# Kernel optimization log

Hardware: AMD Instinct MI355X
Metric: run time of the kernel (lower is better)

Reference implementation:

```python
import jax, jax.numpy as jnp
import numpy as np

B, C, H, NP, M = 32, 768, 12, 196, 64
D = C // H
GRID = 14  # sqrt(196)
NG = 1 + NP  # cls + patches = 197
EPS = 1e-5


def _ln(x, w, b):
    mu = x.mean(-1, keepdims=True)
    var = ((x - mu) ** 2).mean(-1, keepdims=True)
    return (x - mu) * jax.lax.rsqrt(var + EPS) * w + b


def setup_inputs() -> dict:
    key = jax.random.key(0)
    ks = jax.random.split(key, 14)
    std = 0.02
    return {
        "x": jax.random.normal(ks[0], (B, NG + M, C), dtype=jnp.float32),
        "ps": jax.random.uniform(ks[1], (B, M, 2), dtype=jnp.float32) * 224.0,
        "ns": jax.random.randint(ks[2], (B,), 1, M + 1, dtype=jnp.int32),
        "norm1_w": jnp.ones((C,), jnp.float32),
        "norm1_b": jnp.zeros((C,), jnp.float32),
        "qkv_w": jax.random.normal(ks[3], (3 * C, C), jnp.float32) * std,
        "proj_w": jax.random.normal(ks[4], (C, C), jnp.float32) * std,
        "proj_b": jnp.zeros((C,), jnp.float32),
        "norm2_w": jnp.ones((C,), jnp.float32),
        "norm2_b": jnp.zeros((C,), jnp.float32),
        "fc1_w": jax.random.normal(ks[5], (4 * C, C), jnp.float32) * std,
        "fc1_b": jnp.zeros((4 * C,), jnp.float32),
        "fc2_w": jax.random.normal(ks[6], (C, 4 * C), jnp.float32) * std,
        "fc2_b": jnp.zeros((C,), jnp.float32),
    }


def reference(x, ps, ns, norm1_w, norm1_b, qkv_w, proj_w, proj_b,
              norm2_w, norm2_b, fc1_w, fc1_b, fc2_w, fc2_b):
    Bn, Nt, Cd = x.shape  # Nt = 1 + 196 + M
    scale = D ** -0.5

    h = _ln(x, norm1_w, norm1_b)
    qkv = (h @ qkv_w.T).reshape(Bn, Nt, 3, H, D).transpose(2, 0, 3, 1, 4)  # [3,B,H,Nt,D]
    q, k, v = qkv[0], qkv[1], qkv[2]

    # ---- global attention over cls + patch tokens (first 197) ----
    attn = jnp.einsum('bhnd,bhmd->bhnm', q[:, :, :NG], k[:, :, :NG]) * scale
    attn = jax.nn.softmax(attn, axis=-1)
    xg = jnp.einsum('bhnm,bhmd->bhnd', attn, v[:, :, :NG])
    xg = xg.transpose(0, 2, 1, 3).reshape(Bn, NG, Cd)  # [B,197,C]

    # ---- keypoint bilinear-gather attention (get_single_filter_matrix) ----
    pos = ps / 16.0  # [B,M,2]; pos[...,1] -> row (dim 4), pos[...,0] -> col (dim 5)
    c0 = jnp.clip(jnp.floor(pos[..., 0]), 0, GRID - 1).astype(jnp.int32)
    c1 = jnp.clip(jnp.ceil(pos[..., 0]), 0, GRID - 1).astype(jnp.int32)
    r0 = jnp.clip(jnp.floor(pos[..., 1]), 0, GRID - 1).astype(jnp.int32)
    r1 = jnp.clip(jnp.ceil(pos[..., 1]), 0, GRID - 1).astype(jnp.int32)
    # neighbor order: top_left, top_right, bottom_left, bottom_right
    rows = jnp.stack([r0, r1, r0, r1], axis=-1)  # [B,M,4]
    cols = jnp.stack([c0, c0, c1, c1], axis=-1)
    flat = rows * GRID + cols  # [B,M,4] flat index into 196 patch tokens

    kp = k[:, :, 1:NG]  # [B,H,196,D]
    vp = v[:, :, 1:NG]
    idx = jnp.broadcast_to(flat.reshape(Bn, 1, M * 4, 1), (Bn, H, M * 4, D))
    knb = jnp.take_along_axis(kp, idx, axis=2).reshape(Bn, H, M, 4, D)
    vnb = jnp.take_along_axis(vp, idx, axis=2).reshape(Bn, H, M, 4, D)

    qk = q[:, :, NG:]  # keypoint queries [B,H,M,D]
    a = jnp.einsum('bhmd,bhmjd->bhmj', qk, knb)  # no scale, per original
    a = jax.nn.softmax(a, axis=-1)
    kout = jnp.einsum('bhmj,bhmjd->bhmd', a, vnb)
    kout = kout.transpose(0, 2, 1, 3).reshape(Bn, M, Cd)

    y = jnp.concatenate([xg, kout], axis=1) @ proj_w.T + proj_b
    x = x + y

    h2 = _ln(x, norm2_w, norm2_b)
    h2 = jax.nn.gelu(h2 @ fc1_w.T + fc1_b, approximate=False)
    x = x + (h2 @ fc2_w.T + fc2_b)
    return x
```

## Files before the change

### kernel.cpp

```cpp
#include <hip/hip_runtime.h>

typedef unsigned short u16;
typedef unsigned int u32;
typedef u16 u16x8 __attribute__((ext_vector_type(8)));
typedef u16 u16x4 __attribute__((ext_vector_type(4)));
typedef float f32x4 __attribute__((ext_vector_type(4)));
typedef __bf16 bf16x8 __attribute__((ext_vector_type(8)));

#define NHEAD 12
#define NT 261
#define NGL 197
#define CDIM 768
#define KT 14
#define PS_STRIDE 232
#define VT_STRIDE 232

__device__ __forceinline__ float bf2f(u16 u) {
    u32 x = ((u32)u) << 16;
    float f;
    __builtin_memcpy(&f, &x, 4);
    return f;
}
__device__ __forceinline__ u16 f2bf(float f) {
    u32 x;
    __builtin_memcpy(&x, &f, 4);
    x = (x + 0x7fffu + ((x >> 16) & 1u)) >> 16;
    return (u16)x;
}

#define GLD_LDS16(g, l) \
    __builtin_amdgcn_global_load_lds((const __attribute__((address_space(1))) void*)(g), \
                                     (__attribute__((address_space(3))) void*)(l), 16, 0, 0)
#define WAITV(n) asm volatile("s_waitcnt vmcnt(" #n ")" ::: "memory")
#define BARM() asm volatile("s_barrier" ::: "memory")

__global__ __launch_bounds__(256) void convk(const float* __restrict__ in, u16* __restrict__ out, int n4) {
    int i = blockIdx.x * 256 + threadIdx.x;
    if (i >= n4) return;
    float4 v = ((const float4*)in)[i];
    u16x4 o;
    o[0] = f2bf(v.x); o[1] = f2bf(v.y); o[2] = f2bf(v.z); o[3] = f2bf(v.w);
    ((u16x4*)out)[i] = o;
}

__global__ __launch_bounds__(256) void ln_k(const float* __restrict__ in, const float* __restrict__ w,
                                            const float* __restrict__ bia, u16* __restrict__ out) {
    int row = blockIdx.x;
    int tid = threadIdx.x;
    const float* r = in + (size_t)row * CDIM;
    float v0 = r[tid], v1 = r[tid + 256], v2 = r[tid + 512];
    float s = v0 + v1 + v2;
    float ss = v0 * v0 + v1 * v1 + v2 * v2;
#pragma unroll
    for (int off = 32; off; off >>= 1) {
        s += __shfl_xor(s, off);
        ss += __shfl_xor(ss, off);
    }
    __shared__ float ls[4], lss[4];
    int wv = tid >> 6;
    if ((tid & 63) == 0) { ls[wv] = s; lss[wv] = ss; }
    __syncthreads();
    s = ls[0] + ls[1] + ls[2] + ls[3];
    ss = lss[0] + lss[1] + lss[2] + lss[3];
    float mu = s * (1.f / 768.f);
    float var = ss * (1.f / 768.f) - mu * mu;
    float inv = rsqrtf(var + 1e-5f);
    u16* o = out + (size_t)row * CDIM;
    o[tid]       = f2bf((v0 - mu) * inv * w[tid]       + bia[tid]);
    o[tid + 256] = f2bf((v1 - mu) * inv * w[tid + 256] + bia[tid + 256]);
    o[tid + 512] = f2bf((v2 - mu) * inv * w[tid + 512] + bia[tid + 512]);
}

template <int EPI>
__global__ __launch_bounds__(256, 2) void gemm3(const u16* __restrict__ A, const u16* __restrict__ Bw,
                                                int M, int N, int K, int nbn,
                                                const float* __restrict__ bias,
                                                const float* __restrict__ resid, void* __restrict__ outp) {
    __shared__ __align__(16) u16 sm[4][8192];
    const int tid = threadIdx.x;
    const int nwg = gridDim.x;
    const int q = nwg >> 3, r = nwg & 7;
    const int xcd = blockIdx.x & 7, within = blockIdx.x >> 3;
    const int id2 = (xcd < r ? xcd * (q + 1) : r * (q + 1) + (xcd - r) * q) + within;
    const int bm = id2 / nbn, bn = id2 % nbn;
    const int lane = tid & 63, wv = tid >> 6;
    const int wr = wv >> 1, wc = wv & 1;
    const int l15 = lane & 15, lg = lane >> 4;
    const int arow0 = bm * 128, brow0 = bn * 128;
    const int nt = K >> 5;

    const int srow = tid >> 2;
    const int sslot = tid & 3;
    const int sk0 = (sslot ^ ((srow >> 1) & 3)) * 8;
    int arA0 = arow0 + srow;        if (arA0 >= M) arA0 = M - 1;
    int arA1 = arow0 + srow + 64;   if (arA1 >= M) arA1 = M - 1;
    const u16* gA0 = A + (size_t)arA0 * K + sk0;
    const u16* gA1 = A + (size_t)arA1 * K + sk0;
    const u16* gB0 = Bw + (size_t)(brow0 + srow) * K + sk0;
    const u16* gB1 = Bw + (size_t)(brow0 + srow + 64) * K + sk0;
    const int lo0 = tid * 8, lo1 = 2048 + tid * 8;

    auto STAGE = [&](int tt) {
        u16* b = sm[tt & 3];
        const size_t ko = (size_t)tt * 32;
        GLD_LDS16(gA0 + ko, b + lo0);
        GLD_LDS16(gA1 + ko, b + lo1);
        GLD_LDS16(gB0 + ko, b + 4096 + lo0);
        GLD_LDS16(gB1 + ko, b + 4096 + lo1);
    };

    f32x4 acc[4][4] = {};
    const int xorv = (lg ^ ((l15 >> 1) & 3)) << 3;

    STAGE(0); STAGE(1); STAGE(2);
    for (int t = 0; t < nt; ++t) {
        if (t + 2 < nt) { WAITV(8); } else if (t + 1 < nt) { WAITV(4); } else { WAITV(0); }
        BARM();
        if (t + 3 < nt) STAGE(t + 3);
        const u16* bufp = sm[t & 3];
        bf16x8 af[4], bfr[4];
#pragma unroll
        for (int mi = 0; mi < 4; ++mi)
            af[mi] = *(const bf16x8*)(bufp + (wr * 64 + mi * 16 + l15) * 32 + xorv);
#pragma unroll
        for (int ni = 0; ni < 4; ++ni)
            bfr[ni] = *(const bf16x8*)(bufp + 4096 + (wc * 64 + ni * 16 + l15) * 32 + xorv);
#pragma unroll
        for (int mi = 0; mi < 4; ++mi)
#pragma unroll
            for (int ni = 0; ni < 4; ++ni)
                acc[mi][ni] = __builtin_amdgcn_mfma_f32_16x16x32_bf16(af[mi], bfr[ni], acc[mi][ni], 0, 0, 0);
    }

#pragma unroll
    for (int mi = 0; mi < 4; ++mi) {
        int row0 = arow0 + wr * 64 + mi * 16 + lg * 4;
#pragma unroll
        for (int ni = 0; ni < 4; ++ni) {
            int col = brow0 + wc * 64 + ni * 16 + l15;
            float bb = (EPI == 0) ? 0.f : bias[col];
#pragma unroll
            for (int rr = 0; rr < 4; ++rr) {
                int row = row0 + rr;
                if (row < M) {
                    float v = acc[mi][ni][rr] + bb;
                    if (EPI == 2) {
                        float z = v + 0.044715f * v * v * v;
                        v = v / (1.f + __expf(-1.5957691216f * z));
                    }
                    if (EPI == 1) {
                        v += resid[(size_t)row * N + col];
                        ((float*)outp)[(size_t)row * N + col] = v;
                    } else {
                        ((u16*)outp)[(size_t)row * N + col] = f2bf(v);
                    }
                }
            }
        }
    }
}

__global__ __launch_bounds__(256) void attn_global_mfma(const u16* __restrict__ qkv, u16* __restrict__ Z) {
    __shared__ __align__(16) u16 lds0[4 * 16 * PS_STRIDE];
    __shared__ __align__(16) u16 Vt[64 * VT_STRIDE];
    const int tid = threadIdx.x;
    const int blk = blockIdx.x;
    const int qt = blk & 3;
    const int bh = blk >> 2;
    const int h = bh % NHEAD, b = bh / NHEAD;
    const int lane = tid & 63, wv = tid >> 6;
    const int l15 = lane & 15, lg = lane >> 4;
    const u16* base = qkv + (size_t)b * NT * 2304;

    for (int c = tid; c < 224 * 8; c += 256) {
        int row = c >> 3, ch = c & 7;
        u16x8 v = {};
        if (row < NGL) v = *(const u16x8*)(base + (size_t)row * 2304 + 768 + h * 64 + ch * 8);
        int byte = row * 128 + ((ch * 16) ^ ((row & 7) << 4));
        *(u16x8*)((char*)lds0 + byte) = v;
    }
    for (int c = tid; c < 112 * 8; c += 256) {
        int mp = c >> 3, dch = c & 7;
        int m0 = mp * 2;
        u16x8 a0 = {}, a1 = {};
        if (m0 < NGL)     a0 = *(const u16x8*)(base + (size_t)m0 * 2304 + 1536 + h * 64 + dch * 8);
        if (m0 + 1 < NGL) a1 = *(const u16x8*)(base + (size_t)(m0 + 1) * 2304 + 1536 + h * 64 + dch * 8);
#pragma unroll
        for (int j = 0; j < 8; ++j) {
            u32 pk = (u32)a0[j] | ((u32)a1[j] << 16);
            *(u32*)((char*)Vt + (size_t)(dch * 8 + j) * (VT_STRIDE * 2) + m0 * 2) = pk;
        }
    }
    const int q0 = qt * 64 + wv * 16;
    int qrow = q0 + l15; if (qrow > NGL - 1) qrow = NGL - 1;
    bf16x8 aq0 = *(const bf16x8*)(base + (size_t)qrow * 2304 + h * 64 + lg * 8);
    bf16x8 aq1 = *(const bf16x8*)(base + (size_t)qrow * 2304 + h * 64 + 32 + lg * 8);
    __syncthreads();

    f32x4 s[KT];
    const int sw = (l15 & 7) << 4;
#pragma unroll
    for (int t = 0; t < KT; ++t) {
        const char* krow = (const char*)lds0 + (t * 16 + l15) * 128;
        bf16x8 bk0 = *(const bf16x8*)(krow + ((lg * 16) ^ sw));
        bf16x8 bk1 = *(const bf16x8*)(krow + ((64 + lg * 16) ^ sw));
        f32x4 acc = {};
        acc = __builtin_amdgcn_mfma_f32_16x16x32_bf16(aq0, bk0, acc, 0, 0, 0);
        acc = __builtin_amdgcn_mfma_f32_16x16x32_bf16(aq1, bk1, acc, 0, 0, 0);
        s[t] = acc * 0.125f;
    }
    float mx[4] = {-1e30f, -1e30f, -1e30f, -1e30f};
#pragma unroll
    for (int t = 0; t < KT; ++t)
#pragma unroll
        for (int r = 0; r < 4; ++r) mx[r] = fmaxf(mx[r], s[t][r]);
#pragma unroll
    for (int off = 1; off < 16; off <<= 1)
#pragma unroll
        for (int r = 0; r < 4; ++r) mx[r] = fmaxf(mx[r], __shfl_xor(mx[r], off));
    float sum[4] = {};
#pragma unroll
    for (int t = 0; t < KT; ++t) {
        bool valid = (t * 16 + l15) < NGL;
#pragma unroll
        for (int r = 0; r < 4; ++r) {
            float e = valid ? __expf(s[t][r] - mx[r]) : 0.f;
            s[t][r] = e;
            sum[r] += e;
        }
    }
#pragma unroll
    for (int off = 1; off < 16; off <<= 1)
#pragma unroll
        for (int r = 0; r < 4; ++r) sum[r] += __shfl_xor(sum[r], off);
    float inv[4];
#pragma unroll
    for (int r = 0; r < 4; ++r) inv[r] = 1.f / sum[r];

    __syncthreads();
    u16* Pw = lds0 + wv * 16 * PS_STRIDE;
#pragma unroll
    for (int t = 0; t < KT; ++t)
#pragma unroll
        for (int r = 0; r < 4; ++r)
            Pw[(4 * lg + r) * PS_STRIDE + t * 16 + l15] = f2bf(s[t][r] * inv[r]);

    f32x4 o[4] = {};
#pragma unroll
    for (int ks = 0; ks < 7; ++ks) {
        bf16x8 pa = *(const bf16x8*)(Pw + l15 * PS_STRIDE + ks * 32 + lg * 8);
#pragma unroll
        for (int dt = 0; dt < 4; ++dt) {
            bf16x8 bv = *(const bf16x8*)((const char*)Vt + (size_t)(dt * 16 + l15) * (VT_STRIDE * 2) + ks * 64 + lg * 16);
            o[dt] = __builtin_amdgcn_mfma_f32_16x16x32_bf16(pa, bv, o[dt], 0, 0, 0);
        }
    }
#pragma unroll
    for (int dt = 0; dt < 4; ++dt)
#pragma unroll
        for (int r = 0; r < 4; ++r) {
            int q = q0 + 4 * lg + r;
            if (q < NGL) Z[((size_t)b * NT + q) * CDIM + h * 64 + dt * 16 + l15] = f2bf(o[dt][r]);
        }
}

__global__ __launch_bounds__(64) void attn_neigh(const u16* __restrict__ qkv, const float* __restrict__ ps,
                                                 u16* __restrict__ Z) {
    int blk = blockIdx.x;
    int b = blk >> 6, m = blk & 63;
    int lane = threadIdx.x;
    float px = ps[((size_t)b * 64 + m) * 2 + 0] * (1.f / 16.f);
    float py = ps[((size_t)b * 64 + m) * 2 + 1] * (1.f / 16.f);
    int c0 = min(max((int)floorf(px), 0), 13);
    int c1 = min(max((int)ceilf(px), 0), 13);
    int r0 = min(max((int)floorf(py), 0), 13);
    int r1 = min(max((int)ceilf(py), 0), 13);
    int tok[4];
    tok[0] = 1 + r0 * 14 + c0;
    tok[1] = 1 + r1 * 14 + c0;
    tok[2] = 1 + r0 * 14 + c1;
    tok[3] = 1 + r1 * 14 + c1;
    const size_t rowq = ((size_t)b * NT + NGL + m) * 2304;
#pragma unroll 1
    for (int h = 0; h < NHEAD; ++h) {
        float qv = bf2f(qkv[rowq + h * 64 + lane]);
        float a[4];
#pragma unroll
        for (int j = 0; j < 4; ++j) {
            float p = qv * bf2f(qkv[((size_t)b * NT + tok[j]) * 2304 + 768 + h * 64 + lane]);
#pragma unroll
            for (int off = 32; off; off >>= 1) p += __shfl_xor(p, off);
            a[j] = p;
        }
        float mx = fmaxf(fmaxf(a[0], a[1]), fmaxf(a[2], a[3]));
        float e0 = expf(a[0] - mx), e1 = expf(a[1] - mx), e2 = expf(a[2] - mx), e3 = expf(a[3] - mx);
        float inv = 1.f / (e0 + e1 + e2 + e3);
        float v0 = bf2f(qkv[((size_t)b * NT + tok[0]) * 2304 + 1536 + h * 64 + lane]);
        float v1 = bf2f(qkv[((size_t)b * NT + tok[1]) * 2304 + 1536 + h * 64 + lane]);
        float v2 = bf2f(qkv[((size_t)b * NT + tok[2]) * 2304 + 1536 + h * 64 + lane]);
        float v3 = bf2f(qkv[((size_t)b * NT + tok[3]) * 2304 + 1536 + h * 64 + lane]);
        float o = (e0 * v0 + e1 * v1 + e2 * v2 + e3 * v3) * inv;
        Z[((size_t)b * NT + NGL + m) * CDIM + h * 64 + lane] = f2bf(o);
    }
}

extern "C" void kernel_launch(void* const* d_in, const int* in_sizes, int n_in,
                              void* d_out, int out_size, void* d_ws, size_t ws_size,
                              hipStream_t stream) {
    const float* x      = (const float*)d_in[0];
    const float* ps     = (const float*)d_in[1];
    const float* n1w    = (const float*)d_in[3];
    const float* n1b    = (const float*)d_in[4];
    const float* qkv_w  = (const float*)d_in[5];
    const float* proj_w = (const float*)d_in[6];
    const float* proj_b = (const float*)d_in[7];
    const float* n2w    = (const float*)d_in[8];
    const float* n2b    = (const float*)d_in[9];
    const float* fc1_w  = (const float*)d_in[10];
    const float* fc1_b  = (const float*)d_in[11];
    const float* fc2_w  = (const float*)d_in[12];
    const float* fc2_b  = (const float*)d_in[13];

    char* ws = (char*)d_ws;
    const int M = 32 * NT;
    u16* hbuf  = (u16*)ws;
    u16* qkvb  = (u16*)(ws + 12828672);
    u16* Zb    = (u16*)(ws + 12828672 + 38486016);
    u16* Gb    = (u16*)(ws + 12828672);
    float* x1  = (float*)(ws + 64143360);
    u16* wq    = (u16*)(ws + 89800704);
    u16* wp    = wq + 2304 * 768;
    u16* w1    = wp + 768 * 768;
    u16* w2    = w1 + 3072 * 768;

    convk<<<(2304 * 768 / 4 + 255) / 256, 256, 0, stream>>>(qkv_w, wq, 2304 * 768 / 4);
    convk<<<(768 * 768 / 4 + 255) / 256, 256, 0, stream>>>(proj_w, wp, 768 * 768 / 4);
    convk<<<(3072 * 768 / 4 + 255) / 256, 256, 0, stream>>>(fc1_w, w1, 3072 * 768 / 4);
    convk<<<(768 * 3072 / 4 + 255) / 256, 256, 0, stream>>>(fc2_w, w2, 768 * 3072 / 4);

    ln_k<<<M, 256, 0, stream>>>(x, n1w, n1b, hbuf);
    gemm3<0><<<66 * 18, 256, 0, stream>>>(hbuf, wq, M, 2304, 768, 18, nullptr, nullptr, qkvb);
    attn_global_mfma<<<32 * NHEAD * 4, 256, 0, stream>>>(qkvb, Zb);
    attn_neigh<<<32 * 64, 64, 0, stream>>>(qkvb, ps, Zb);
    gemm3<1><<<66 * 6, 256, 0, stream>>>(Zb, wp, M, 768, 768, 6, proj_b, x, x1);
    ln_k<<<M, 256, 0, stream>>>(x1, n2w, n2b, hbuf);
    gemm3<2><<<66 * 24, 256, 0, stream>>>(hbuf, w1, M, 3072, 768, 24, fc1_b, nullptr, Gb);
    gemm3<1><<<66 * 6, 256, 0, stream>>>(Gb, w2, M, 768, 3072, 6, fc2_b, x1, (float*)d_out);
}
```

Before: 322.6 us.

## Rework GEMM to BK=64 double-buffered tiles with 256-row variant; batch weight conversions

The GEMM is replaced by a templated version that loads K tiles of 64 instead of 32 and uses two LDS buffers instead of four. The XOR swizzle now spans 8 slots. For the QKV and fc1 GEMMs, a 256-row M tile with 512 threads is used, so each weight tile is reused across more rows. The four fp32-to-bf16 weight conversion launches are merged into one 2D-grid launch to reduce launch overhead. Dropping to double buffering with an extra barrier per iteration may expose more load latency, and the larger blocks lower per-CU occupancy.

```diff
diff --git a/kernel.cpp b/kernel.cpp
--- a/kernel.cpp
+++ b/kernel.cpp
@@ -34,7 +34,16 @@
 #define WAITV(n) asm volatile("s_waitcnt vmcnt(" #n ")" ::: "memory")
 #define BARM() asm volatile("s_barrier" ::: "memory")
 
-__global__ __launch_bounds__(256) void convk(const float* __restrict__ in, u16* __restrict__ out, int n4) {
+struct CvArgs {
+    const float* in[4];
+    u16* out[4];
+    int n4[4];
+};
+__global__ __launch_bounds__(256) void convk4(CvArgs a) {
+    int y = blockIdx.y;
+    const float* in = a.in[y];
+    u16* out = a.out[y];
+    int n4 = a.n4[y];
     int i = blockIdx.x * 256 + threadIdx.x;
     if (i >= n4) return;
     float4 v = ((const float4*)in)[i];
@@ -71,12 +80,16 @@
     o[tid + 512] = f2bf((v2 - mu) * inv * w[tid + 512] + bia[tid + 512]);
 }
 
-template <int EPI>
-__global__ __launch_bounds__(256, 2) void gemm3(const u16* __restrict__ A, const u16* __restrict__ Bw,
-                                                int M, int N, int K, int nbn,
-                                                const float* __restrict__ bias,
-                                                const float* __restrict__ resid, void* __restrict__ outp) {
-    __shared__ __align__(16) u16 sm[4][8192];
+template <int EPI, int TM>
+__global__ __launch_bounds__(TM * 2, 2) void gemm4(const u16* __restrict__ A, const u16* __restrict__ Bw,
+                                                   int M, int N, int K, int nbn,
+                                                   const float* __restrict__ bias,
+                                                   const float* __restrict__ resid, void* __restrict__ outp) {
+    constexpr int THREADS = TM * 2;
+    constexpr int ROWSP = THREADS / 8;
+    constexpr int NBI = 128 / ROWSP;
+    constexpr int SLOT = TM * 64 + 8192;
+    __shared__ __align__(16) u16 sm[2 * SLOT];
     const int tid = threadIdx.x;
     const int nwg = gridDim.x;
     const int q = nwg >> 3, r = nwg & 7;
@@ -86,50 +99,64 @@
     const int lane = tid & 63, wv = tid >> 6;
     const int wr = wv >> 1, wc = wv & 1;
     const int l15 = lane & 15, lg = lane >> 4;
-    const int arow0 = bm * 128, brow0 = bn * 128;
-    const int nt = K >> 5;
-
-    const int srow = tid >> 2;
-    const int sslot = tid & 3;
-    const int sk0 = (sslot ^ ((srow >> 1) & 3)) * 8;
-    int arA0 = arow0 + srow;        if (arA0 >= M) arA0 = M - 1;
-    int arA1 = arow0 + srow + 64;   if (arA1 >= M) arA1 = M - 1;
-    const u16* gA0 = A + (size_t)arA0 * K + sk0;
-    const u16* gA1 = A + (size_t)arA1 * K + sk0;
-    const u16* gB0 = Bw + (size_t)(brow0 + srow) * K + sk0;
-    const u16* gB1 = Bw + (size_t)(brow0 + srow + 64) * K + sk0;
-    const int lo0 = tid * 8, lo1 = 2048 + tid * 8;
+    const int arow0 = bm * TM, brow0 = bn * 128;
+    const int nt = K >> 6;
+
+    const int srow = tid >> 3;
+    const int sk = ((tid & 7) ^ (srow & 7)) * 8;
+    const u16* gA[4];
+    const u16* gB[NBI];
+#pragma unroll
+    for (int i = 0; i < 4; ++i) {
+        int ar = arow0 + i * ROWSP + srow;
+        if (ar >= M) ar = M - 1;
+        gA[i] = A + (size_t)ar * K + sk;
+    }
+#pragma unroll
+    for (int j = 0; j < NBI; ++j)
+        gB[j] = Bw + (size_t)(brow0 + j * ROWSP + srow) * K + sk;
 
     auto STAGE = [&](int tt) {
-        u16* b = sm[tt & 3];
-        const size_t ko = (size_t)tt * 32;
-        GLD_LDS16(gA0 + ko, b + lo0);
-        GLD_LDS16(gA1 + ko, b + lo1);
-        GLD_LDS16(gB0 + ko, b + 4096 + lo0);
-        GLD_LDS16(gB1 + ko, b + 4096 + lo1);
+        u16* sb = sm + (tt & 1) * SLOT;
+        const size_t ko = (size_t)tt * 64;
+#pragma unroll
+        for (int i = 0; i < 4; ++i) GLD_LDS16(gA[i] + ko, sb + i * (ROWSP * 64) + tid * 8);
+#pragma unroll
+        for (int j = 0; j < NBI; ++j) GLD_LDS16(gB[j] + ko, sb + TM * 64 + j * (ROWSP * 64) + tid * 8);
     };
 
     f32x4 acc[4][4] = {};
-    const int xorv = (lg ^ ((l15 >> 1) & 3)) << 3;
-
-    STAGE(0); STAGE(1); STAGE(2);
+    const int xb = l15 & 7;
+
+    STAGE(0);
     for (int t = 0; t < nt; ++t) {
-        if (t + 2 < nt) { WAITV(8); } else if (t + 1 < nt) { WAITV(4); } else { WAITV(0); }
+        if (t + 1 < nt) {
+            STAGE(t + 1);
+            if constexpr (TM == 256) { WAITV(6); } else { WAITV(8); }
+        } else {
+            WAITV(0);
+        }
         BARM();
-        if (t + 3 < nt) STAGE(t + 3);
-        const u16* bufp = sm[t & 3];
-        bf16x8 af[4], bfr[4];
+        const u16* sb = sm + (t & 1) * SLOT;
+        bf16x8 af[4][2], bq[4][2];
 #pragma unroll
         for (int mi = 0; mi < 4; ++mi)
-            af[mi] = *(const bf16x8*)(bufp + (wr * 64 + mi * 16 + l15) * 32 + xorv);
+#pragma unroll
+            for (int kk = 0; kk < 2; ++kk)
+                af[mi][kk] = *(const bf16x8*)(sb + (wr * 64 + mi * 16 + l15) * 64 + (((kk << 2) | lg) ^ xb) * 8);
 #pragma unroll
         for (int ni = 0; ni < 4; ++ni)
-            bfr[ni] = *(const bf16x8*)(bufp + 4096 + (wc * 64 + ni * 16 + l15) * 32 + xorv);
+#pragma unroll
+            for (int kk = 0; kk < 2; ++kk)
+                bq[ni][kk] = *(const bf16x8*)(sb + TM * 64 + (wc * 64 + ni * 16 + l15) * 64 + (((kk << 2) | lg) ^ xb) * 8);
 #pragma unroll
         for (int mi = 0; mi < 4; ++mi)
 #pragma unroll
-            for (int ni = 0; ni < 4; ++ni)
-                acc[mi][ni] = __builtin_amdgcn_mfma_f32_16x16x32_bf16(af[mi], bfr[ni], acc[mi][ni], 0, 0, 0);
+            for (int ni = 0; ni < 4; ++ni) {
+                acc[mi][ni] = __builtin_amdgcn_mfma_f32_16x16x32_bf16(af[mi][0], bq[ni][0], acc[mi][ni], 0, 0, 0);
+                acc[mi][ni] = __builtin_amdgcn_mfma_f32_16x16x32_bf16(af[mi][1], bq[ni][1], acc[mi][ni], 0, 0, 0);
+            }
+        if (t + 2 < nt) BARM();
     }
 
 #pragma unroll
@@ -333,17 +360,19 @@
     u16* w1    = wp + 768 * 768;
     u16* w2    = w1 + 3072 * 768;
 
-    convk<<<(2304 * 768 / 4 + 255) / 256, 256, 0, stream>>>(qkv_w, wq, 2304 * 768 / 4);
-    convk<<<(768 * 768 / 4 + 255) / 256, 256, 0, stream>>>(proj_w, wp, 768 * 768 / 4);
-    convk<<<(3072 * 768 / 4 + 255) / 256, 256, 0, stream>>>(fc1_w, w1, 3072 * 768 / 4);
-    convk<<<(768 * 3072 / 4 + 255) / 256, 256, 0, stream>>>(fc2_w, w2, 768 * 3072 / 4);
+    CvArgs cv;
+    cv.in[0] = qkv_w;  cv.out[0] = wq; cv.n4[0] = 2304 * 768 / 4;
+    cv.in[1] = proj_w; cv.out[1] = wp; cv.n4[1] = 768 * 768 / 4;
+    cv.in[2] = fc1_w;  cv.out[2] = w1; cv.n4[2] = 3072 * 768 / 4;
+    cv.in[3] = fc2_w;  cv.out[3] = w2; cv.n4[3] = 768 * 3072 / 4;
+    convk4<<<dim3((3072 * 768 / 4 + 255) / 256, 4), 256, 0, stream>>>(cv);
 
     ln_k<<<M, 256, 0, stream>>>(x, n1w, n1b, hbuf);
-    gemm3<0><<<66 * 18, 256, 0, stream>>>(hbuf, wq, M, 2304, 768, 18, nullptr, nullptr, qkvb);
+    gemm4<0, 256><<<33 * 18, 512, 0, stream>>>(hbuf, wq, M, 2304, 768, 18, nullptr, nullptr, qkvb);
     attn_global_mfma<<<32 * NHEAD * 4, 256, 0, stream>>>(qkvb, Zb);
     attn_neigh<<<32 * 64, 64, 0, stream>>>(qkvb, ps, Zb);
-    gemm3<1><<<66 * 6, 256, 0, stream>>>(Zb, wp, M, 768, 768, 6, proj_b, x, x1);
+    gemm4<1, 128><<<66 * 6, 256, 0, stream>>>(Zb, wp, M, 768, 768, 6, proj_b, x, x1);
     ln_k<<<M, 256, 0, stream>>>(x1, n2w, n2b, hbuf);
-    gemm3<2><<<66 * 24, 256, 0, stream>>>(hbuf, w1, M, 3072, 768, 24, fc1_b, nullptr, Gb);
-    gemm3<1><<<66 * 6, 256, 0, stream>>>(Gb, w2, M, 768, 3072, 6, fc2_b, x1, (float*)d_out);
-}
+    gemm4<2, 256><<<33 * 24, 512, 0, stream>>>(hbuf, w1, M, 3072, 768, 24, fc1_b, nullptr, Gb);
+    gemm4<1, 128><<<66 * 6, 256, 0, stream>>>(Gb, w2, M, 768, 3072, 6, fc2_b, x1, (float*)d_out);
+}
```

After: 309.1 us. 1.04x faster.
